# Kernel optimization log

Hardware: AMD Instinct MI355X
Metric: run time of the kernel (lower is better)

The kernel has to match this reference:

```python
import jax, jax.numpy as jnp
import numpy as np

TEMP = 1.0          # temperature
BASE_TEMP = 0.5     # base_temperature
TOPK = 200          # hard-negative mining top-k
BSZ, NVIEWS, D = 4096, 1, 128
NUM_CLASSES = 100


def setup_inputs() -> dict:
    key = jax.random.key(0)
    k1, k2 = jax.random.split(key)
    feats = jax.random.normal(k1, (BSZ, NVIEWS, D), dtype=jnp.float32)
    feats = feats / jnp.linalg.norm(feats, axis=-1, keepdims=True)  # unit-norm embeddings
    labels = jax.random.randint(k2, (BSZ,), 0, NUM_CLASSES)  # label 0 rows are excluded as anchors
    return {"features": feats, "labels": labels}


def _supcon_topk(features, labels):
    bsz = features.shape[0]
    # n_views == 1, contrast_mode == 'all': anchor == contrast == features[:, 0]
    f = features.reshape(bsz, -1)                          # [B, D]
    lab = labels.reshape(-1)
    mask = (lab[:, None] == lab[None, :]).astype(jnp.float32)   # [B, B] same-class mask
    logits_mask = 1.0 - jnp.eye(bsz, dtype=jnp.float32)         # remove self-contrast

    adc = jnp.matmul(f, f.T) / TEMP                             # anchor . contrast^T
    logits_max = jax.lax.stop_gradient(jnp.max(adc, axis=1, keepdims=True))  # .detach()
    logits = (adc - logits_max) * 10.0

    pos_mask = mask * logits_mask
    neg_mask = 1.0 - mask
    exp_logits = jnp.exp(logits) * logits_mask
    neg_exp = exp_logits * neg_mask

    # top-k hard negatives per anchor row -> scatter into a 0/1 mask
    _, ind = jax.lax.top_k(neg_exp, TOPK)                       # [B, TOPK]
    mask_topk = jnp.zeros_like(mask).at[jnp.arange(bsz)[:, None], ind].set(1.0)
    all_mask = pos_mask + mask_topk

    denom = jnp.sum(exp_logits * all_mask, axis=1, keepdims=True)
    log_prob = logits - jnp.log(denom)

    pos_cnt = jnp.sum(pos_mask, axis=1)
    # row selection in the torch code: anchors with label > 0 AND at least one positive.
    valid = (lab > 0) & (pos_cnt > 0)
    mean_log_prob_pos = jnp.sum(pos_mask * log_prob, axis=1) / jnp.where(pos_cnt > 0, pos_cnt, 1.0)
    per_row = -(TEMP / BASE_TEMP) * mean_log_prob_pos
    return jnp.sum(jnp.where(valid, per_row, 0.0)) / jnp.sum(valid).astype(jnp.float32)


def reference(features, labels):
    return _supcon_topk(features, labels)
```

## Files before the change

### kernel.cpp

```cpp
#include <hip/hip_runtime.h>
#include <math.h>

#define BSZ 4096
#define DIM 128
#define K_TOP 200
#define TGUESS 0.11f
#define HBINS 512

typedef unsigned short u16;
typedef unsigned int u32;
typedef __attribute__((ext_vector_type(8))) short bf16x8;
typedef __attribute__((ext_vector_type(4))) float floatx4;

__device__ inline u16 f2bf(float x) {
    u32 u = __float_as_uint(x);
    return (u16)((u + 0x7fffu + ((u >> 16) & 1u)) >> 16);
}

__global__ __launch_bounds__(256) void pre_kernel(const float* __restrict__ F,
                                                  u16* __restrict__ Fb) {
    int idx = blockIdx.x * 256 + threadIdx.x;
    if (idx < BSZ * DIM / 4) {
        float4 v = ((const float4*)F)[idx];
        ushort4 r;
        r.x = f2bf(v.x); r.y = f2bf(v.y); r.z = f2bf(v.z); r.w = f2bf(v.w);
        ((ushort4*)Fb)[idx] = r;
    }
}

__global__ __launch_bounds__(1024) void fused_all(const u16* __restrict__ Fb,
                                                  const int* __restrict__ labels,
                                                  float2* __restrict__ rowout) {
    __shared__ int   hcnt[16 * HBINS];
    __shared__ float hexp[16 * HBINS];
    __shared__ unsigned char labc[BSZ];
    __shared__ float ps[16], pe[16], pc[16];

    const int tid  = threadIdx.x;
    const int wave = tid >> 6, lane = tid & 63;
    const int l16  = lane & 15, quad = lane >> 4;
    const int brow = blockIdx.x * 16;

    {
        int4 lv = ((const int4*)labels)[tid];
        uchar4 r;
        r.x = (unsigned char)lv.x; r.y = (unsigned char)lv.y;
        r.z = (unsigned char)lv.z; r.w = (unsigned char)lv.w;
        ((uchar4*)labc)[tid] = r;
    }
    #pragma unroll
    for (int q = 0; q < 8; ++q) { hcnt[q * 1024 + tid] = 0; hexp[q * 1024 + tid] = 0.f; }
    if (tid < 16) { ps[tid] = 0.f; pe[tid] = 0.f; pc[tid] = 0.f; }
    __syncthreads();

    const u16* Ab = Fb + (size_t)(brow + l16) * DIM + quad * 8;
    bf16x8 afr[4];
    #pragma unroll
    for (int ks = 0; ks < 4; ++ks) afr[ks] = *(const bf16x8*)(Ab + ks * 32);

    unsigned char labr_[4];
    #pragma unroll
    for (int e = 0; e < 4; ++e) labr_[e] = labc[brow + quad * 4 + e];

    for (int t = 0; t < 8; ++t) {
        const int tn0 = wave * 256 + t * 32;
        const u16* B0 = Fb + (size_t)(tn0 + l16) * DIM + quad * 8;
        const u16* B1 = Fb + (size_t)(tn0 + 16 + l16) * DIM + quad * 8;
        floatx4 a0 = (floatx4){0.f, 0.f, 0.f, 0.f};
        floatx4 a1 = (floatx4){0.f, 0.f, 0.f, 0.f};
        #pragma unroll
        for (int ks = 0; ks < 4; ++ks) {
            bf16x8 b0 = *(const bf16x8*)(B0 + ks * 32);
            bf16x8 b1 = *(const bf16x8*)(B1 + ks * 32);
            a0 = __builtin_amdgcn_mfma_f32_16x16x32_bf16(afr[ks], b0, a0, 0, 0, 0);
            a1 = __builtin_amdgcn_mfma_f32_16x16x32_bf16(afr[ks], b1, a1, 0, 0, 0);
        }
        #pragma unroll
        for (int nt = 0; nt < 2; ++nt) {
            const floatx4 accv = nt ? a1 : a0;
            const int cg_ = tn0 + nt * 16 + l16;
            const int lc = labc[cg_];
            #pragma unroll
            for (int e = 0; e < 4; ++e) {
                const int rl = quad * 4 + e;
                const int rg = brow + rl;
                if (cg_ == rg) continue;
                const float s = accv[e];
                if (lc == (int)labr_[e]) {
                    atomicAdd(&ps[rl], s);
                    atomicAdd(&pe[rl], __expf((s - 1.f) * 10.f));
                    atomicAdd(&pc[rl], 1.f);
                } else if (s > TGUESS) {
                    int b = (int)((s - 0.1f) * 800.f);
                    b = b < 0 ? 0 : (b > HBINS - 1 ? HBINS - 1 : b);
                    const float ex = __expf((s - 1.f) * 10.f);
                    atomicAdd(&hcnt[rl * HBINS + b], 1);
                    atomicAdd(&hexp[rl * HBINS + b], ex);
                }
            }
        }
    }
    __syncthreads();

    {
        const int r = wave;
        const int* hc = hcnt + r * HBINS;
        const float* hx = hexp + r * HBINS;

        int local[8], csum = 0;
        #pragma unroll
        for (int t2 = 0; t2 < 8; ++t2) { local[t2] = hc[lane * 8 + t2]; csum += local[t2]; }
        int suf = csum;
        #pragma unroll
        for (int off = 1; off < 64; off <<= 1) {
            int t2 = __shfl_down(suf, off);
            if (lane + off < 64) suf += t2;
        }
        const int above = suf - csum;
        const bool owner = (above < K_TOP) && (suf >= K_TOP);
        int b1o = 0, c1o = 0;
        if (owner) {
            int acc2 = above;
            #pragma unroll
            for (int t2 = 7; t2 >= 0; --t2) {
                if (acc2 + local[t2] >= K_TOP) { b1o = lane * 8 + t2; c1o = acc2; break; }
                acc2 += local[t2];
            }
        }
        unsigned long long bm = __ballot(owner);
        int b1, K2;
        if (bm == 0ull) {
            b1 = -1; K2 = 0;
        } else {
            const int src = __ffsll((long long)bm) - 1;
            b1 = __shfl(b1o, src);
            K2 = K_TOP - __shfl(c1o, src);
        }

        float te = 0.f;
        #pragma unroll
        for (int t2 = 0; t2 < 8; ++t2) {
            const int b = lane * 8 + t2;
            if (b > b1) te += hx[b];
        }
        #pragma unroll
        for (int off = 32; off; off >>= 1) te += __shfl_down(te, off);

        if (lane == 0) {
            float tsum = 0.f;
            if (K2 > 0) {
                const int cb = hc[b1];
                if (cb > 0) tsum = (float)K2 * hx[b1] / (float)cb;
            }
            const float pcnt = pc[r];
            const int labi = labc[brow + r];
            float pr = 0.f, vd = 0.f;
            if (labi > 0 && pcnt > 0.f) {
                float denom = pe[r] + te + tsum;
                float slp = 10.f * (ps[r] - pcnt) - pcnt * logf(denom);
                pr = -2.f * slp / pcnt;
                vd = 1.f;
            }
            rowout[brow + r] = make_float2(pr, vd);
        }
    }
}

__global__ __launch_bounds__(256) void reduce_kernel(const float2* __restrict__ rowout,
                                                     float* __restrict__ out) {
    __shared__ float reda[4], redb[4];
    const int tid = threadIdx.x, lane = tid & 63, w = tid >> 6;
    float sa = 0.f, sb = 0.f;
    #pragma unroll
    for (int j = 0; j < 16; ++j) {
        float2 v = rowout[j * 256 + tid];
        sa += v.x; sb += v.y;
    }
    #pragma unroll
    for (int off = 32; off; off >>= 1) {
        sa += __shfl_down(sa, off);
        sb += __shfl_down(sb, off);
    }
    if (lane == 0) { reda[w] = sa; redb[w] = sb; }
    __syncthreads();
    if (tid == 0)
        out[0] = (reda[0] + reda[1] + reda[2] + reda[3]) /
                 (redb[0] + redb[1] + redb[2] + redb[3]);
}

extern "C" void kernel_launch(void* const* d_in, const int* in_sizes, int n_in,
                              void* d_out, int out_size, void* d_ws, size_t ws_size,
                              hipStream_t stream) {
    const float* F      = (const float*)d_in[0];
    const int*   labels = (const int*)d_in[1];
    float*       out    = (float*)d_out;

    char* w = (char*)d_ws;
    u16*    Fb     = (u16*)w;               w += (size_t)BSZ * DIM * 2;
    float2* rowout = (float2*)w;            w += (size_t)BSZ * 8;

    pre_kernel<<<512, 256, 0, stream>>>(F, Fb);
    fused_all<<<256, 1024, 0, stream>>>(Fb, labels, rowout);
    reduce_kernel<<<1, 256, 0, stream>>>(rowout, out);
}
```

Measured before the change: 95.09 us.

## Split column range across two blocks and fuse final reduction into top-k kernel

The fused GEMM+histogram kernel is split so each 16-row tile is processed by two blocks, each covering half of the columns. Per-half histograms and positive statistics are written to global memory. A second kernel merges them and performs the top-k threshold selection. The separate final reduce launch is replaced by a last-block-done atomic counter inside that second kernel. This aims to double the block count for better CU occupancy on 256-CU hardware, at the cost of writing and reading about 32 MB of histogram traffic through global memory.

```diff
diff --git a/kernel.cpp b/kernel.cpp
--- a/kernel.cpp
+++ b/kernel.cpp
@@ -6,6 +6,7 @@
 #define K_TOP 200
 #define TGUESS 0.11f
 #define HBINS 512
+#define NBLK2 256
 
 typedef unsigned short u16;
 typedef unsigned int u32;
@@ -18,7 +19,8 @@
 }
 
 __global__ __launch_bounds__(256) void pre_kernel(const float* __restrict__ F,
-                                                  u16* __restrict__ Fb) {
+                                                  u16* __restrict__ Fb,
+                                                  int* __restrict__ done) {
     int idx = blockIdx.x * 256 + threadIdx.x;
     if (idx < BSZ * DIM / 4) {
         float4 v = ((const float4*)F)[idx];
@@ -26,46 +28,55 @@
         r.x = f2bf(v.x); r.y = f2bf(v.y); r.z = f2bf(v.z); r.w = f2bf(v.w);
         ((ushort4*)Fb)[idx] = r;
     }
-}
-
-__global__ __launch_bounds__(1024) void fused_all(const u16* __restrict__ Fb,
-                                                  const int* __restrict__ labels,
-                                                  float2* __restrict__ rowout) {
+    if (idx == 0) done[0] = 0;
+}
+
+__global__ __launch_bounds__(1024, 8) void gemm_half(const u16* __restrict__ Fb,
+                                                     const int* __restrict__ labels,
+                                                     int* __restrict__ ghcnt,
+                                                     float* __restrict__ ghexp,
+                                                     float4* __restrict__ gstat) {
     __shared__ int   hcnt[16 * HBINS];
     __shared__ float hexp[16 * HBINS];
-    __shared__ unsigned char labc[BSZ];
+    __shared__ unsigned char labh[2048];
+    __shared__ unsigned char labr8[16];
     __shared__ float ps[16], pe[16], pc[16];
 
     const int tid  = threadIdx.x;
     const int wave = tid >> 6, lane = tid & 63;
     const int l16  = lane & 15, quad = lane >> 4;
-    const int brow = blockIdx.x * 16;
-
-    {
-        int4 lv = ((const int4*)labels)[tid];
+    const int rg0  = (blockIdx.x >> 1) * 16;
+    const int half = blockIdx.x & 1;
+    const int c0   = half * 2048;
+
+    if (tid < 512) {
+        int4 lv = ((const int4*)(labels + c0))[tid];
         uchar4 r;
         r.x = (unsigned char)lv.x; r.y = (unsigned char)lv.y;
         r.z = (unsigned char)lv.z; r.w = (unsigned char)lv.w;
-        ((uchar4*)labc)[tid] = r;
+        ((uchar4*)labh)[tid] = r;
     }
     #pragma unroll
     for (int q = 0; q < 8; ++q) { hcnt[q * 1024 + tid] = 0; hexp[q * 1024 + tid] = 0.f; }
-    if (tid < 16) { ps[tid] = 0.f; pe[tid] = 0.f; pc[tid] = 0.f; }
-    __syncthreads();
-
-    const u16* Ab = Fb + (size_t)(brow + l16) * DIM + quad * 8;
+    if (tid < 16) {
+        ps[tid] = 0.f; pe[tid] = 0.f; pc[tid] = 0.f;
+        labr8[tid] = (unsigned char)labels[rg0 + tid];
+    }
+    __syncthreads();
+
+    const u16* Ab = Fb + (size_t)(rg0 + l16) * DIM + quad * 8;
     bf16x8 afr[4];
     #pragma unroll
     for (int ks = 0; ks < 4; ++ks) afr[ks] = *(const bf16x8*)(Ab + ks * 32);
 
     unsigned char labr_[4];
     #pragma unroll
-    for (int e = 0; e < 4; ++e) labr_[e] = labc[brow + quad * 4 + e];
-
-    for (int t = 0; t < 8; ++t) {
-        const int tn0 = wave * 256 + t * 32;
-        const u16* B0 = Fb + (size_t)(tn0 + l16) * DIM + quad * 8;
-        const u16* B1 = Fb + (size_t)(tn0 + 16 + l16) * DIM + quad * 8;
+    for (int e = 0; e < 4; ++e) labr_[e] = labr8[quad * 4 + e];
+
+    for (int t = 0; t < 4; ++t) {
+        const int cl0 = wave * 128 + t * 32;
+        const u16* B0 = Fb + (size_t)(c0 + cl0 + l16) * DIM + quad * 8;
+        const u16* B1 = Fb + (size_t)(c0 + cl0 + 16 + l16) * DIM + quad * 8;
         floatx4 a0 = (floatx4){0.f, 0.f, 0.f, 0.f};
         floatx4 a1 = (floatx4){0.f, 0.f, 0.f, 0.f};
         #pragma unroll
@@ -78,12 +89,13 @@
         #pragma unroll
         for (int nt = 0; nt < 2; ++nt) {
             const floatx4 accv = nt ? a1 : a0;
-            const int cg_ = tn0 + nt * 16 + l16;
-            const int lc = labc[cg_];
+            const int cl = cl0 + nt * 16 + l16;
+            const int cg_ = c0 + cl;
+            const int lc = labh[cl];
             #pragma unroll
             for (int e = 0; e < 4; ++e) {
                 const int rl = quad * 4 + e;
-                const int rg = brow + rl;
+                const int rg = rg0 + rl;
                 if (cg_ == rg) continue;
                 const float s = accv[e];
                 if (lc == (int)labr_[e]) {
@@ -102,6 +114,45 @@
     }
     __syncthreads();
 
+    #pragma unroll
+    for (int q8 = 0; q8 < 8; ++q8) {
+        const int q = q8 * 1024 + tid;
+        const int row = q >> 9, bin = q & 511;
+        const size_t g = ((size_t)(rg0 + row) * 2 + half) * HBINS + bin;
+        ghcnt[g] = hcnt[q];
+        ghexp[g] = hexp[q];
+    }
+    if (tid < 16)
+        gstat[(size_t)(rg0 + tid) * 2 + half] =
+            make_float4(ps[tid], pe[tid], pc[tid], 0.f);
+}
+
+__global__ __launch_bounds__(1024) void topk_finish(const int* __restrict__ ghcnt,
+                                                    const float* __restrict__ ghexp,
+                                                    const float4* __restrict__ gstat,
+                                                    const int* __restrict__ labels,
+                                                    float2* __restrict__ rowout,
+                                                    int* __restrict__ done,
+                                                    float* __restrict__ out) {
+    __shared__ int   hcnt[16 * HBINS];
+    __shared__ float hexp[16 * HBINS];
+    __shared__ float reda[16], redb[16];
+    __shared__ int   lastflag;
+
+    const int tid = threadIdx.x, wave = tid >> 6, lane = tid & 63;
+    const int brow = blockIdx.x * 16;
+
+    #pragma unroll
+    for (int q8 = 0; q8 < 8; ++q8) {
+        const int q = q8 * 1024 + tid;
+        const int row = q >> 9, bin = q & 511;
+        const size_t g0 = ((size_t)(brow + row) * 2 + 0) * HBINS + bin;
+        const size_t g1 = ((size_t)(brow + row) * 2 + 1) * HBINS + bin;
+        hcnt[q] = ghcnt[g0] + ghcnt[g1];
+        hexp[q] = ghexp[g0] + ghexp[g1];
+    }
+    __syncthreads();
+
     {
         const int r = wave;
         const int* hc = hcnt + r * HBINS;
@@ -129,9 +180,8 @@
         }
         unsigned long long bm = __ballot(owner);
         int b1, K2;
-        if (bm == 0ull) {
-            b1 = -1; K2 = 0;
-        } else {
+        if (bm == 0ull) { b1 = -1; K2 = 0; }
+        else {
             const int src = __ffsll((long long)bm) - 1;
             b1 = __shfl(b1o, src);
             K2 = K_TOP - __shfl(c1o, src);
@@ -148,44 +198,54 @@
 
         if (lane == 0) {
             float tsum = 0.f;
-            if (K2 > 0) {
+            if (K2 > 0 && b1 >= 0) {
                 const int cb = hc[b1];
                 if (cb > 0) tsum = (float)K2 * hx[b1] / (float)cb;
             }
-            const float pcnt = pc[r];
-            const int labi = labc[brow + r];
+            float4 g0 = gstat[(size_t)(brow + r) * 2 + 0];
+            float4 g1 = gstat[(size_t)(brow + r) * 2 + 1];
+            const float psum = g0.x + g1.x, pexp = g0.y + g1.y, pcnt = g0.z + g1.z;
+            const int labi = labels[brow + r];
             float pr = 0.f, vd = 0.f;
             if (labi > 0 && pcnt > 0.f) {
-                float denom = pe[r] + te + tsum;
-                float slp = 10.f * (ps[r] - pcnt) - pcnt * logf(denom);
+                float denom = pexp + te + tsum;
+                float slp = 10.f * (psum - pcnt) - pcnt * logf(denom);
                 pr = -2.f * slp / pcnt;
                 vd = 1.f;
             }
             rowout[brow + r] = make_float2(pr, vd);
         }
     }
-}
-
-__global__ __launch_bounds__(256) void reduce_kernel(const float2* __restrict__ rowout,
-                                                     float* __restrict__ out) {
-    __shared__ float reda[4], redb[4];
-    const int tid = threadIdx.x, lane = tid & 63, w = tid >> 6;
-    float sa = 0.f, sb = 0.f;
-    #pragma unroll
-    for (int j = 0; j < 16; ++j) {
-        float2 v = rowout[j * 256 + tid];
-        sa += v.x; sb += v.y;
-    }
-    #pragma unroll
-    for (int off = 32; off; off >>= 1) {
-        sa += __shfl_down(sa, off);
-        sb += __shfl_down(sb, off);
-    }
-    if (lane == 0) { reda[w] = sa; redb[w] = sb; }
-    __syncthreads();
-    if (tid == 0)
-        out[0] = (reda[0] + reda[1] + reda[2] + reda[3]) /
-                 (redb[0] + redb[1] + redb[2] + redb[3]);
+
+    __syncthreads();
+    if (tid == 0) {
+        __threadfence();
+        int old = atomicAdd(done, 1);
+        lastflag = (old == NBLK2 - 1);
+    }
+    __syncthreads();
+    if (lastflag) {
+        __threadfence();
+        float sa = 0.f, sb = 0.f;
+        #pragma unroll
+        for (int j = 0; j < 4; ++j) {
+            float2 v2 = rowout[j * 1024 + tid];
+            sa += v2.x; sb += v2.y;
+        }
+        #pragma unroll
+        for (int off = 32; off; off >>= 1) {
+            sa += __shfl_down(sa, off);
+            sb += __shfl_down(sb, off);
+        }
+        if (lane == 0) { reda[wave] = sa; redb[wave] = sb; }
+        __syncthreads();
+        if (tid == 0) {
+            float ta = 0.f, tb = 0.f;
+            #pragma unroll
+            for (int q = 0; q < 16; ++q) { ta += reda[q]; tb += redb[q]; }
+            out[0] = ta / tb;
+        }
+    }
 }
 
 extern "C" void kernel_launch(void* const* d_in, const int* in_sizes, int n_in,
@@ -196,10 +256,14 @@
     float*       out    = (float*)d_out;
 
     char* w = (char*)d_ws;
-    u16*    Fb     = (u16*)w;               w += (size_t)BSZ * DIM * 2;
-    float2* rowout = (float2*)w;            w += (size_t)BSZ * 8;
-
-    pre_kernel<<<512, 256, 0, stream>>>(F, Fb);
-    fused_all<<<256, 1024, 0, stream>>>(Fb, labels, rowout);
-    reduce_kernel<<<1, 256, 0, stream>>>(rowout, out);
-}
+    u16*    Fb     = (u16*)w;    w += (size_t)BSZ * DIM * 2;
+    int*    ghcnt  = (int*)w;    w += (size_t)BSZ * 2 * HBINS * 4;
+    float*  ghexp  = (float*)w;  w += (size_t)BSZ * 2 * HBINS * 4;
+    float4* gstat  = (float4*)w; w += (size_t)BSZ * 2 * 16;
+    float2* rowout = (float2*)w; w += (size_t)BSZ * 8;
+    int*    done   = (int*)w;    w += 64;
+
+    pre_kernel<<<512, 256, 0, stream>>>(F, Fb, done);
+    gemm_half<<<512, 1024, 0, stream>>>(Fb, labels, ghcnt, ghexp, gstat);
+    topk_finish<<<NBLK2, 1024, 0, stream>>>(ghcnt, ghexp, gstat, labels, rowout, done, out);
+}
```

New measurement: 122.1 us. +28.4%, slower.
